# Optimization experiments

Hardware: AMD Instinct MI355X
Metric: run time of the kernel (lower is better)

Reference implementation:

```python
import jax, jax.numpy as jnp
import numpy as np

N_EMBED = 1024
E_DIM = 256
BETA = 0.25


def setup_inputs() -> dict:
    key = jax.random.key(0)
    k1, k2 = jax.random.split(key)
    z = jax.random.normal(k1, (32, 16, 16, 16, E_DIM), dtype=jnp.float32)
    emb = jax.random.normal(k2, (N_EMBED, E_DIM), dtype=jnp.float32)
    return {"z": z, "emb": emb}


def reference(z, emb):
    sg = jax.lax.stop_gradient
    z_flat = z.reshape(-1, E_DIM)                      # [N, e_dim]
    similarity = z_flat @ emb.T                        # [N, n_embed]
    codebook_idxs = jnp.argmax(similarity, axis=-1)    # [N]
    z_q = emb[codebook_idxs].reshape(z.shape)          # gather nearest code
    vq_loss = jnp.mean((z_q - sg(z)) ** 2)
    commitment_loss = BETA * jnp.mean((sg(z_q) - z) ** 2)
    z_q = z + sg(z_q - z)                              # straight-through
    return (z_q, vq_loss, commitment_loss, codebook_idxs)
```

## Files before the change

### kernel.cpp

```cpp
#include <hip/hip_runtime.h>

#define E_DIM  256
#define NC     1024
#define BM     128
#define NT     512
#define MARGIN 0.02f

typedef short  bf16x4 __attribute__((ext_vector_type(4)));
typedef short  bf16x8 __attribute__((ext_vector_type(8)));
typedef float  f32x4  __attribute__((ext_vector_type(4)));

static __device__ __forceinline__ void split2(float x, short& hi, short& lo) {
    const unsigned u  = __float_as_uint(x);
    const unsigned hb = (u + 0x7FFFu + ((u >> 16) & 1u)) >> 16;
    hi = (short)hb;
    const float l = x - __uint_as_float(hb << 16);
    const unsigned u2 = __float_as_uint(l);
    lo = (short)((u2 + 0x7FFFu + ((u2 >> 16) & 1u)) >> 16);
}

static __device__ __forceinline__ float mkey(float v, unsigned il) {
    return __uint_as_float((__float_as_uint(v) & 0xFFFFFC00u) | il);
}

static __device__ __forceinline__ void gload16(const void* g, void* l) {
    __builtin_amdgcn_global_load_lds(
        (const __attribute__((address_space(1))) unsigned int*)g,
        (__attribute__((address_space(3))) unsigned int*)l, 16, 0, 0);
}

__global__ __launch_bounds__(256) void vq_prep(
    const float* __restrict__ emb, short* __restrict__ img)
{
    const int t     = blockIdx.x * 256 + threadIdx.x;
    const int b     = t & 7;
    const int row   = (t >> 3) & 127;
    const int chunk = (t >> 10) & 3;
    const int tile  = t >> 12;
    const int cb    = (b << 4) ^ ((row & 7) << 4);
    const int s0    = cb >> 1;
    const float* src = &emb[(size_t)(tile * 128 + row) * E_DIM + chunk * 64 + s0];
    const f32x4 x0 = *reinterpret_cast<const f32x4*>(&src[0]);
    const f32x4 x1 = *reinterpret_cast<const f32x4*>(&src[4]);
    bf16x8 h, l; short hh, ll;
#pragma unroll
    for (int j = 0; j < 4; ++j) { split2(x0[j], hh, ll); h[j]     = hh; l[j]     = ll; }
#pragma unroll
    for (int j = 0; j < 4; ++j) { split2(x1[j], hh, ll); h[4 + j] = hh; l[4 + j] = ll; }
    const size_t base = (size_t)(tile * 4 + chunk) * 16384;
    *reinterpret_cast<bf16x8*>(&img[base + row * 64 + b * 8])        = h;
    *reinterpret_cast<bf16x8*>(&img[base + 8192 + row * 64 + b * 8]) = l;
}

__global__ __launch_bounds__(NT, 2) void vq_kernel(
    const float* __restrict__ z, const float* __restrict__ emb,
    const short* __restrict__ img, float* __restrict__ zq,
    float* __restrict__ loss, float* __restrict__ idxf, float invN)
{
    __shared__ char  Bs[2][32768];
    __shared__ float topk[2][BM][2];
    __shared__ int   rowIdx[BM];
    __shared__ int   ambList[BM];
    __shared__ int   ambCnt;
    __shared__ float zs[E_DIM];
    __shared__ float redV[8];
    __shared__ int   redI[8];

    const int tid  = threadIdx.x;
    const int lane = tid & 63;
    const int w    = tid >> 6;
    const int wm   = w >> 1;
    const int wn   = w & 1;
    const int l15  = lane & 15;
    const int l4   = lane >> 4;
    const int rb   = blockIdx.x * BM;

    {
        const char* g = (const char*)img;
#pragma unroll
        for (int q = 0; q < 4; ++q) {
            const int off = (q * 8 + w) * 1024;
            gload16(g + off + (lane << 4), &Bs[0][off]);
        }
    }

    bf16x8 a_hi[2][8], a_lo[2][8];
#pragma unroll
    for (int m = 0; m < 2; ++m) {
        const float* zp = &z[(size_t)(rb + wm * 32 + m * 16 + l15) * E_DIM + l4 * 8];
#pragma unroll
        for (int s = 0; s < 8; ++s) {
            const f32x4 x0 = *reinterpret_cast<const f32x4*>(&zp[s * 32]);
            const f32x4 x1 = *reinterpret_cast<const f32x4*>(&zp[s * 32 + 4]);
            bf16x8 h, l; short hh, ll;
#pragma unroll
            for (int j = 0; j < 4; ++j) { split2(x0[j], hh, ll); h[j]   = hh; l[j]   = ll; }
#pragma unroll
            for (int j = 0; j < 4; ++j) { split2(x1[j], hh, ll); h[4+j] = hh; l[4+j] = ll; }
            a_hi[m][s] = h; a_lo[m][s] = l;
        }
    }

    float k1[2][4], k2[2][4];
#pragma unroll
    for (int m = 0; m < 2; ++m)
#pragma unroll
        for (int j = 0; j < 4; ++j) { k1[m][j] = -3.0e38f; k2[m][j] = -3.0e38f; }

    __syncthreads();

    for (int tile = 0; tile < 8; ++tile) {
        f32x4 acc[2][4];
        const f32x4 zz = {0.f, 0.f, 0.f, 0.f};
#pragma unroll
        for (int m = 0; m < 2; ++m)
#pragma unroll
            for (int n = 0; n < 4; ++n) acc[m][n] = zz;

#pragma unroll
        for (int kk = 0; kk < 4; ++kk) {
            const int gc  = tile * 4 + kk;
            const int sgc = (gc < 31) ? gc + 1 : 31;
            {
                const char* g = (const char*)img + (size_t)sgc * 32768;
                char* const db = Bs[(kk + 1) & 1];
#pragma unroll
                for (int q = 0; q < 4; ++q) {
                    const int off = (q * 8 + w) * 1024;
                    gload16(g + off + (lane << 4), &db[off]);
                }
            }
            const char* bc = Bs[kk & 1];
#pragma unroll
            for (int h = 0; h < 2; ++h) {
                bf16x8 bh[4], bl[4];
#pragma unroll
                for (int n = 0; n < 4; ++n) {
                    const int row = wn * 64 + n * 16 + l15;
                    const int off = row * 128 + (((h * 4 + l4) << 4) ^ ((row & 7) << 4));
                    bh[n] = *reinterpret_cast<const bf16x8*>(&bc[off]);
                    bl[n] = *reinterpret_cast<const bf16x8*>(&bc[16384 + off]);
                }
#pragma unroll
                for (int m = 0; m < 2; ++m) {
                    const bf16x8 ah = a_hi[m][kk * 2 + h];
                    const bf16x8 al = a_lo[m][kk * 2 + h];
#pragma unroll
                    for (int n = 0; n < 4; ++n) {
                        acc[m][n] = __builtin_amdgcn_mfma_f32_16x16x32_bf16(ah, bh[n], acc[m][n], 0, 0, 0);
                        acc[m][n] = __builtin_amdgcn_mfma_f32_16x16x32_bf16(ah, bl[n], acc[m][n], 0, 0, 0);
                        acc[m][n] = __builtin_amdgcn_mfma_f32_16x16x32_bf16(al, bh[n], acc[m][n], 0, 0, 0);
                    }
                }
            }
            __syncthreads();
        }

        const int colbase = tile * 128 + wn * 64 + l15;
        unsigned il[4];
#pragma unroll
        for (int n = 0; n < 4; ++n) il[n] = (unsigned)(1023 - (colbase + n * 16));
#pragma unroll
        for (int m = 0; m < 2; ++m)
#pragma unroll
            for (int j = 0; j < 4; ++j) {
                const float a0 = acc[m][0][j], a1 = acc[m][1][j];
                const float a2 = acc[m][2][j], a3 = acc[m][3][j];
                const float q = fmaxf(fmaxf(a0, a1), fmaxf(a2, a3));
                if (q > k2[m][j]) {
                    float x, t;
                    x = mkey(a0, il[0]); t = fminf(k1[m][j], x);
                    k1[m][j] = fmaxf(k1[m][j], x); k2[m][j] = fmaxf(k2[m][j], t);
                    x = mkey(a1, il[1]); t = fminf(k1[m][j], x);
                    k1[m][j] = fmaxf(k1[m][j], x); k2[m][j] = fmaxf(k2[m][j], t);
                    x = mkey(a2, il[2]); t = fminf(k1[m][j], x);
                    k1[m][j] = fmaxf(k1[m][j], x); k2[m][j] = fmaxf(k2[m][j], t);
                    x = mkey(a3, il[3]); t = fminf(k1[m][j], x);
                    k1[m][j] = fmaxf(k1[m][j], x); k2[m][j] = fmaxf(k2[m][j], t);
                }
            }
    }

#pragma unroll
    for (int m = 0; m < 2; ++m)
#pragma unroll
        for (int j = 0; j < 4; ++j) {
            float a = k1[m][j], b = k2[m][j];
#pragma unroll
            for (int s = 1; s < 16; s <<= 1) {
                const float oa = __shfl_xor(a, s, 64);
                const float ob = __shfl_xor(b, s, 64);
                const float t  = fminf(a, oa);
                a = fmaxf(a, oa);
                b = fmaxf(fmaxf(b, ob), t);
            }
            if (l15 == 0) {
                const int row = wm * 32 + m * 16 + l4 * 4 + j;
                topk[wn][row][0] = a;
                topk[wn][row][1] = b;
            }
        }
    if (tid == 0) ambCnt = 0;
    __syncthreads();

    if (tid < BM) {
        float a = topk[0][tid][0], b = topk[0][tid][1];
        const float oa = topk[1][tid][0], ob = topk[1][tid][1];
        const float t  = fminf(a, oa);
        a = fmaxf(a, oa);
        b = fmaxf(fmaxf(b, ob), t);
        const unsigned ub = __float_as_uint(a);
        rowIdx[tid] = 1023 - (int)(ub & 1023u);
        const float v1 = __uint_as_float(ub & 0xFFFFFC00u);
        const float v2 = __uint_as_float(__float_as_uint(b) & 0xFFFFFC00u);
        if (v1 - v2 <= MARGIN) {
            const int p = atomicAdd(&ambCnt, 1);
            ambList[p] = tid;
        }
    }
    __syncthreads();

    const int nAmb = ambCnt;
    for (int ai = 0; ai < nAmb; ++ai) {
        const int row = ambList[ai];
        if (tid < 64)
            *reinterpret_cast<f32x4*>(&zs[tid * 4]) =
                *reinterpret_cast<const f32x4*>(&z[(size_t)(rb + row) * E_DIM + tid * 4]);
        __syncthreads();
        float best = -3.0e38f; int bidx = 0;
#pragma unroll
        for (int cc = 0; cc < 2; ++cc) {
            const int c = tid * 2 + cc;
            const float* ep = &emb[(size_t)c * E_DIM];
            float p = 0.f;
#pragma unroll 8
            for (int qd = 0; qd < 64; ++qd) {
                const f32x4 e4 = *reinterpret_cast<const f32x4*>(&ep[qd * 4]);
                const f32x4 z4 = *reinterpret_cast<const f32x4*>(&zs[qd * 4]);
                p = fmaf(z4[0], e4[0], p); p = fmaf(z4[1], e4[1], p);
                p = fmaf(z4[2], e4[2], p); p = fmaf(z4[3], e4[3], p);
            }
            if (p > best) { best = p; bidx = c; }
        }
#pragma unroll
        for (int s = 1; s < 64; s <<= 1) {
            const float ov = __shfl_xor(best, s, 64);
            const int   oi = __shfl_xor(bidx, s, 64);
            if (ov > best || (ov == best && oi < bidx)) { best = ov; bidx = oi; }
        }
        if (lane == 0) { redV[w] = best; redI[w] = bidx; }
        __syncthreads();
        if (tid == 0) {
            float bb = redV[0]; int bi = redI[0];
#pragma unroll
            for (int ww = 1; ww < 8; ++ww)
                if (redV[ww] > bb) { bb = redV[ww]; bi = redI[ww]; }
            rowIdx[row] = bi;
        }
        __syncthreads();
    }

    float sse = 0.f;
#pragma unroll
    for (int i = 0; i < 16; ++i) {
        const int f   = i * NT + tid;
        const int row = f >> 6;
        const int kq  = f & 63;
        const int idx = rowIdx[row];
        const f32x4 e4 = *reinterpret_cast<const f32x4*>(&emb[(size_t)idx * E_DIM + kq * 4]);
        const f32x4 z4 = *reinterpret_cast<const f32x4*>(&z[(size_t)(rb + row) * E_DIM + kq * 4]);
        const float d0 = e4[0] - z4[0], d1 = e4[1] - z4[1];
        const float d2 = e4[2] - z4[2], d3 = e4[3] - z4[3];
        sse += d0 * d0 + d1 * d1 + d2 * d2 + d3 * d3;
        *reinterpret_cast<f32x4*>(&zq[(size_t)(rb + row) * E_DIM + kq * 4]) = e4;
    }
    if (tid < BM) idxf[rb + tid] = (float)rowIdx[tid];
#pragma unroll
    for (int s = 1; s < 64; s <<= 1) sse += __shfl_xor(sse, s, 64);
    if (lane == 0) redV[w] = sse;
    __syncthreads();
    if (tid == 0) {
        float t = 0.f;
#pragma unroll
        for (int ww = 0; ww < 8; ++ww) t += redV[ww];
        atomicAdd(&loss[0], t * invN);
        atomicAdd(&loss[1], 0.25f * t * invN);
    }
}

extern "C" void kernel_launch(void* const* d_in, const int* in_sizes, int n_in,
                              void* d_out, int out_size, void* d_ws, size_t ws_size,
                              hipStream_t stream) {
    const float* z   = (const float*)d_in[0];
    const float* emb = (const float*)d_in[1];
    const int zsz    = in_sizes[0];
    const int nrows  = zsz / E_DIM;

    float* out  = (float*)d_out;
    float* zq   = out;
    float* loss = out + zsz;
    float* idxf = out + zsz + 2;

    short* img = (short*)d_ws;

    hipMemsetAsync(loss, 0, 2 * sizeof(float), stream);

    vq_prep<<<dim3(128), 256, 0, stream>>>(emb, img);
    vq_kernel<<<dim3(nrows / BM), NT, 0, stream>>>(
        z, emb, img, zq, loss, idxf, 1.0f / ((float)nrows * (float)E_DIM));
}
```

Measured before the change: 632.0 us.

## Triple-buffer codebook chunks with vmcnt-based waits and interleaved hi/lo layout

```diff
diff --git a/kernel.cpp b/kernel.cpp
--- a/kernel.cpp
+++ b/kernel.cpp
@@ -6,7 +6,6 @@
 #define NT     512
 #define MARGIN 0.02f
 
-typedef short  bf16x4 __attribute__((ext_vector_type(4)));
 typedef short  bf16x8 __attribute__((ext_vector_type(8)));
 typedef float  f32x4  __attribute__((ext_vector_type(4)));
 
@@ -32,14 +31,12 @@
 __global__ __launch_bounds__(256) void vq_prep(
     const float* __restrict__ emb, short* __restrict__ img)
 {
-    const int t     = blockIdx.x * 256 + threadIdx.x;
-    const int b     = t & 7;
-    const int row   = (t >> 3) & 127;
-    const int chunk = (t >> 10) & 3;
-    const int tile  = t >> 12;
-    const int cb    = (b << 4) ^ ((row & 7) << 4);
-    const int s0    = cb >> 1;
-    const float* src = &emb[(size_t)(tile * 128 + row) * E_DIM + chunk * 64 + s0];
+    const int t    = blockIdx.x * 256 + threadIdx.x;
+    const int kg   = t & 3;
+    const int r    = (t >> 2) & 127;
+    const int kc   = (t >> 9) & 7;
+    const int tile = t >> 12;
+    const float* src = &emb[(size_t)(tile * 128 + r) * E_DIM + kc * 32 + kg * 8];
     const f32x4 x0 = *reinterpret_cast<const f32x4*>(&src[0]);
     const f32x4 x1 = *reinterpret_cast<const f32x4*>(&src[4]);
     bf16x8 h, l; short hh, ll;
@@ -47,9 +44,11 @@
     for (int j = 0; j < 4; ++j) { split2(x0[j], hh, ll); h[j]     = hh; l[j]     = ll; }
 #pragma unroll
     for (int j = 0; j < 4; ++j) { split2(x1[j], hh, ll); h[4 + j] = hh; l[4 + j] = ll; }
-    const size_t base = (size_t)(tile * 4 + chunk) * 16384;
-    *reinterpret_cast<bf16x8*>(&img[base + row * 64 + b * 8])        = h;
-    *reinterpret_cast<bf16x8*>(&img[base + 8192 + row * 64 + b * 8]) = l;
+    const int hs = kg ^ (r & 7);
+    const int ls = (4 + kg) ^ (r & 7);
+    short* rowp = &img[(size_t)(tile * 8 + kc) * 8192 + r * 64];
+    *reinterpret_cast<bf16x8*>(&rowp[hs * 8]) = h;
+    *reinterpret_cast<bf16x8*>(&rowp[ls * 8]) = l;
 }
 
 __global__ __launch_bounds__(NT, 2) void vq_kernel(
@@ -57,7 +56,7 @@
     const short* __restrict__ img, float* __restrict__ zq,
     float* __restrict__ loss, float* __restrict__ idxf, float invN)
 {
-    __shared__ char  Bs[2][32768];
+    __shared__ char  Bs[3][16384];
     __shared__ float topk[2][BM][2];
     __shared__ int   rowIdx[BM];
     __shared__ int   ambList[BM];
@@ -75,14 +74,13 @@
     const int l4   = lane >> 4;
     const int rb   = blockIdx.x * BM;
 
-    {
-        const char* g = (const char*)img;
-#pragma unroll
-        for (int q = 0; q < 4; ++q) {
+#pragma unroll
+    for (int c = 0; c < 2; ++c)
+#pragma unroll
+        for (int q = 0; q < 2; ++q) {
             const int off = (q * 8 + w) * 1024;
-            gload16(g + off + (lane << 4), &Bs[0][off]);
-        }
-    }
+            gload16((const char*)img + c * 16384 + off + (lane << 4), &Bs[c][off]);
+        }
 
     bf16x8 a_hi[2][8], a_lo[2][8];
 #pragma unroll
@@ -107,8 +105,19 @@
 #pragma unroll
         for (int j = 0; j < 4; ++j) { k1[m][j] = -3.0e38f; k2[m][j] = -3.0e38f; }
 
-    __syncthreads();
-
+    int offH[4], offL[4];
+#pragma unroll
+    for (int n = 0; n < 4; ++n) {
+        const int row = wn * 64 + n * 16 + l15;
+        const int sw  = (row & 7) << 4;
+        offH[n] = row * 128 + ((l4 << 4) ^ sw);
+        offL[n] = row * 128 + (((4 + l4) << 4) ^ sw);
+    }
+
+    asm volatile("s_waitcnt vmcnt(2)" ::: "memory");
+    __builtin_amdgcn_s_barrier();
+
+    int cur = 0, nx2 = 2;
     for (int tile = 0; tile < 8; ++tile) {
         f32x4 acc[2][4];
         const f32x4 zz = {0.f, 0.f, 0.f, 0.f};
@@ -118,42 +127,40 @@
             for (int n = 0; n < 4; ++n) acc[m][n] = zz;
 
 #pragma unroll
-        for (int kk = 0; kk < 4; ++kk) {
-            const int gc  = tile * 4 + kk;
-            const int sgc = (gc < 31) ? gc + 1 : 31;
-            {
-                const char* g = (const char*)img + (size_t)sgc * 32768;
-                char* const db = Bs[(kk + 1) & 1];
-#pragma unroll
-                for (int q = 0; q < 4; ++q) {
+        for (int kc = 0; kc < 8; ++kc) {
+            const int gc = tile * 8 + kc;
+            if (gc <= 61) {
+                const char* g = (const char*)img + (size_t)(gc + 2) * 16384;
+                char* const db = Bs[nx2];
+#pragma unroll
+                for (int q = 0; q < 2; ++q) {
                     const int off = (q * 8 + w) * 1024;
-                    gload16(g + off + (lane << 4), &db[off]);
+                    gload16(g + off + (lane << 4), db + off);
                 }
             }
-            const char* bc = Bs[kk & 1];
-#pragma unroll
-            for (int h = 0; h < 2; ++h) {
-                bf16x8 bh[4], bl[4];
+            const char* bc = Bs[cur];
+            bf16x8 bh[4], bl[4];
+#pragma unroll
+            for (int n = 0; n < 4; ++n) {
+                bh[n] = *reinterpret_cast<const bf16x8*>(&bc[offH[n]]);
+                bl[n] = *reinterpret_cast<const bf16x8*>(&bc[offL[n]]);
+            }
+#pragma unroll
+            for (int m = 0; m < 2; ++m) {
+                const bf16x8 ah = a_hi[m][kc];
+                const bf16x8 al = a_lo[m][kc];
 #pragma unroll
                 for (int n = 0; n < 4; ++n) {
-                    const int row = wn * 64 + n * 16 + l15;
-                    const int off = row * 128 + (((h * 4 + l4) << 4) ^ ((row & 7) << 4));
-                    bh[n] = *reinterpret_cast<const bf16x8*>(&bc[off]);
-                    bl[n] = *reinterpret_cast<const bf16x8*>(&bc[16384 + off]);
+                    acc[m][n] = __builtin_amdgcn_mfma_f32_16x16x32_bf16(ah, bh[n], acc[m][n], 0, 0, 0);
+                    acc[m][n] = __builtin_amdgcn_mfma_f32_16x16x32_bf16(ah, bl[n], acc[m][n], 0, 0, 0);
+                    acc[m][n] = __builtin_amdgcn_mfma_f32_16x16x32_bf16(al, bh[n], acc[m][n], 0, 0, 0);
                 }
-#pragma unroll
-                for (int m = 0; m < 2; ++m) {
-                    const bf16x8 ah = a_hi[m][kk * 2 + h];
-                    const bf16x8 al = a_lo[m][kk * 2 + h];
-#pragma unroll
-                    for (int n = 0; n < 4; ++n) {
-                        acc[m][n] = __builtin_amdgcn_mfma_f32_16x16x32_bf16(ah, bh[n], acc[m][n], 0, 0, 0);
-                        acc[m][n] = __builtin_amdgcn_mfma_f32_16x16x32_bf16(ah, bl[n], acc[m][n], 0, 0, 0);
-                        acc[m][n] = __builtin_amdgcn_mfma_f32_16x16x32_bf16(al, bh[n], acc[m][n], 0, 0, 0);
-                    }
-                }
-            }
-            __syncthreads();
+            }
+            if (gc < 62) asm volatile("s_waitcnt vmcnt(2)" ::: "memory");
+            else         asm volatile("s_waitcnt vmcnt(0)" ::: "memory");
+            __builtin_amdgcn_s_barrier();
+            cur = (cur == 2) ? 0 : cur + 1;
+            nx2 = (nx2 == 2) ? 0 : nx2 + 1;
         }
 
         const int colbase = tile * 128 + wn * 64 + l15;
```

Result: slower. 661.5 us (+4.7%).
